# Performance work log

Measured on AMD Instinct MI355X. Metric: run time of the kernel, lower is better.

## Reference

```python
import jax, jax.numpy as jnp
import numpy as np

NUM_HEADS = 16
CAPACITY = 512
ROPE_BASE = 10000.0

def _rope_factor(positions, dim):
    # freqs = exp(linspace(0,-1,dim//2) * log(base)), shape (dim//2,)
    freqs = jnp.exp(jnp.linspace(0.0, -1.0, dim // 2) * jnp.log(jnp.float32(ROPE_BASE)))
    angles = positions[..., None] * freqs            # (..., seq, dim//2)
    return jnp.concatenate([jnp.sin(angles), jnp.cos(angles)], axis=-1)  # (..., seq, dim)

def setup_inputs() -> dict:
    key = jax.random.key(0)
    ks = jax.random.split(key, 6)
    B, Sq, Skv, D = 4, 4096, 4096, 1024
    return {
        "query_seq": jax.random.normal(ks[0], (B, Sq, D), jnp.float32),
        "value_seq": jax.random.normal(ks[1], (B, Skv, D), jnp.float32),
        "router_w": jax.random.normal(ks[2], (1, D), jnp.float32) * 0.02,
        "q_w": jax.random.normal(ks[3], (D, D), jnp.float32) * 0.02,
        "kv_w": jax.random.normal(ks[4], (2 * D, D), jnp.float32) * 0.02,
        "out_w": jax.random.normal(ks[5], (D, D), jnp.float32) * 0.02,
    }

def reference(query_seq, value_seq, router_w, q_w, kv_w, out_w):
    B, Sq, D = query_seq.shape
    Skv = value_seq.shape[1]
    H, C = NUM_HEADS, CAPACITY
    d = D // H

    # router + top-k capacity selection over the sequence dim
    rw = jnp.einsum("bsd,od->bs", query_seq, router_w).astype(jnp.float32)  # (B,Sq)
    top_w, top_idx = jax.lax.top_k(rw, C)                                   # (B,C)

    # gather selected queries
    resampled = jnp.take_along_axis(query_seq, top_idx[:, :, None], axis=1)  # (B,C,D)

    q = jnp.einsum("bcd,ed->bce", resampled, q_w)        # (B,C,H*d)
    kv = jnp.einsum("bsd,ed->bse", value_seq, kv_w)      # (B,Skv,2*H*d)
    k, v = jnp.split(kv, 2, axis=-1)

    q = q.reshape(B, C, H, d).transpose(0, 2, 1, 3)      # (B,H,C,d)
    k = k.reshape(B, Skv, H, d).transpose(0, 2, 1, 3)    # (B,H,Skv,d)
    v = v.reshape(B, Skv, H, d).transpose(0, 2, 1, 3)

    # RoPE-style elementwise modulation (faithful to source: x * cat(sin, cos))
    q_pos = top_idx.astype(jnp.float32)[:, None, :]      # (B,1,C)
    q = q * _rope_factor(q_pos, d)                       # (B,H,C,d)
    k_pos = jnp.arange(Skv, dtype=jnp.float32)[None, :]  # (1,Skv)
    k = k * _rope_factor(k_pos, d)[None]                 # broadcast over (B,H)

    # SDPA
    scores = jnp.einsum("bhcd,bhsd->bhcs", q, k) / jnp.sqrt(jnp.float32(d))
    att = jnp.einsum("bhcs,bhsd->bhcd", jax.nn.softmax(scores, axis=-1), v)

    att = att.transpose(0, 2, 1, 3).reshape(B, C, H * d)  # (B,C,D)
    att = jnp.einsum("bce,de->bcd", att, out_w)           # (B,C,D)

    # weighted scatter back to full sequence
    src = att * top_w[:, :, None]
    out = jnp.zeros_like(query_seq).at[jnp.arange(B)[:, None], top_idx].set(src)
    return out
```

## Files before the change

### kernel.cpp

```cpp
#include <hip/hip_runtime.h>
#include <hip/hip_bf16.h>

#define B_  4
#define SQ  4096
#define SKV 4096
#define DM  1024
#define NH  16
#define HD  64
#define CAP 512

#define ASPLIT 4
#define KVPER  (SKV / ASPLIT)
#define AITERS (KVPER / 64)

typedef __attribute__((ext_vector_type(8))) short    short8;
typedef __attribute__((ext_vector_type(8))) __bf16   bf16v8;
typedef __attribute__((ext_vector_type(4))) float    f32x4;
typedef __attribute__((ext_vector_type(4))) unsigned short ushort4v;

static __device__ __forceinline__ unsigned short f2bf(float f) {
    unsigned u = __float_as_uint(f);
    u += 0x7FFFu + ((u >> 16) & 1u);
    return (unsigned short)(u >> 16);
}

static __device__ __forceinline__ f32x4 mfma_bf16(short8 a, short8 b, f32x4 c) {
    return __builtin_amdgcn_mfma_f32_16x16x32_bf16(
        __builtin_bit_cast(bf16v8, a), __builtin_bit_cast(bf16v8, b), c, 0, 0, 0);
}

#define GLD16(gp, lp)                                                              \
    __builtin_amdgcn_global_load_lds(                                              \
        (__attribute__((address_space(1))) void*)(gp),                             \
        (__attribute__((address_space(3))) void*)(lp), 16, 0, 0)

__global__ void __launch_bounds__(256) k_convert(const float* __restrict__ in,
                                                 unsigned short* __restrict__ out) {
    size_t i = (size_t)blockIdx.x * 256 + threadIdx.x;
    float4 f = ((const float4*)in)[i];
    ushort4v o = { f2bf(f.x), f2bf(f.y), f2bf(f.z), f2bf(f.w) };
    ((ushort4v*)out)[i] = o;
}

__global__ void __launch_bounds__(256) k_rope(float* __restrict__ tab) {
    int g = blockIdx.x * 256 + threadIdx.x;
    int pos = g >> 6, i = g & 63, j = i & 31;
    float freq = expf(-(float)j * (logf(10000.0f) / 31.0f));
    float ang  = (float)pos * freq;
    tab[g] = (i < 32) ? sinf(ang) : cosf(ang);
}

__global__ void __launch_bounds__(256) k_router(const float* __restrict__ q,
                                                const float* __restrict__ wv,
                                                float* __restrict__ rw) {
    int row  = blockIdx.x * 4 + (threadIdx.x >> 6);
    int lane = threadIdx.x & 63;
    const float* p  = q  + (size_t)row * DM + lane * 16;
    const float* wp = wv + lane * 16;
    float s = 0.f;
#pragma unroll
    for (int j = 0; j < 4; j++) {
        float4 a = ((const float4*)p)[j];
        float4 b = ((const float4*)wp)[j];
        s += a.x * b.x + a.y * b.y + a.z * b.z + a.w * b.w;
    }
#pragma unroll
    for (int m = 32; m > 0; m >>= 1) s += __shfl_xor(s, m, 64);
    if (lane == 0) rw[row] = s;
}

__global__ void __launch_bounds__(1024) k_topk(const float* __restrict__ rw,
                                               int* __restrict__ sel,
                                               float* __restrict__ selw) {
    __shared__ unsigned long long keys[4096];
    int b = blockIdx.x, t = threadIdx.x;
    for (int i = t; i < 4096; i += 1024) {
        float v = rw[b * 4096 + i];
        unsigned u = __float_as_uint(v);
        u = (u & 0x80000000u) ? ~u : (u | 0x80000000u);
        keys[i] = ((unsigned long long)(~u) << 32) | (unsigned)i;
    }
    __syncthreads();
    for (int k = 2; k <= 4096; k <<= 1)
        for (int j = k >> 1; j > 0; j >>= 1) {
            for (int i = t; i < 4096; i += 1024) {
                int ixj = i ^ j;
                if (ixj > i) {
                    bool up = ((i & k) == 0);
                    unsigned long long a = keys[i], c = keys[ixj];
                    if ((a > c) == up) { keys[i] = c; keys[ixj] = a; }
                }
            }
            __syncthreads();
        }
    for (int i = t; i < 512; i += 1024) {
        unsigned idx = (unsigned)(keys[i] & 0xFFFFFFFFu);
        sel[b * 512 + i]  = (int)idx;
        selw[b * 512 + i] = rw[b * 4096 + idx];
    }
}

__global__ void __launch_bounds__(256) k_gather(const float* __restrict__ q,
                                                const int* __restrict__ sel,
                                                unsigned short* __restrict__ out) {
    int row = blockIdx.x;
    int b = row >> 9;
    int s = sel[row];
    const float4* src = (const float4*)(q + ((size_t)b * SQ + s) * DM);
    ushort4v* dst = (ushort4v*)(out + (size_t)row * DM);
    float4 f = src[threadIdx.x];
    ushort4v o = { f2bf(f.x), f2bf(f.y), f2bf(f.z), f2bf(f.w) };
    dst[threadIdx.x] = o;
}

template <int MODE, int BN>
__global__ void __launch_bounds__(256) k_gemm(
    const unsigned short* __restrict__ A,
    const unsigned short* __restrict__ Bw,
    int M, int N, int K,
    const float* __restrict__ rope_tab,
    const int* __restrict__ sel,
    const float* __restrict__ selw,
    unsigned short* __restrict__ ok,
    unsigned short* __restrict__ ov,
    unsigned short* __restrict__ obf,
    float* __restrict__ of) {
    constexpr int TN = BN / 32;
    __shared__ unsigned short lA[128 * 32];
    __shared__ unsigned short lB[BN * 32];
    const int tid = threadIdx.x;
    const int w = tid >> 6, lane = tid & 63, quad = lane >> 4, l16 = lane & 15;
    const int wr = w >> 1, wc = w & 1;
    const int mBase = blockIdx.y * 128;
    const int nBase = blockIdx.x * BN + (MODE == 3 ? 1024 : 0);

    f32x4 acc[4][TN] = {};

    for (int k0 = 0; k0 < K; k0 += 32) {
#pragma unroll
        for (int is = 0; is < 2; is++) {
            int slot = is * 256 + tid;
            int row = slot >> 2, sc = slot & 3;
            int kc = (sc - (row >> 1)) & 3;
            const char* ga = (const char*)A + (((size_t)(mBase + row) * K) + k0 + kc * 8) * 2;
            GLD16(ga, (char*)lA + slot * 16);
        }
#pragma unroll
        for (int is = 0; is < BN / 64; is++) {
            int slot = is * 256 + tid;
            int row = slot >> 2, sc = slot & 3;
            int kc = (sc - (row >> 1)) & 3;
            const char* gb = (const char*)Bw + (((size_t)(nBase + row) * K) + k0 + kc * 8) * 2;
            GLD16(gb, (char*)lB + slot * 16);
        }
        __syncthreads();
        short8 af[4], bfr[TN];
#pragma unroll
        for (int t = 0; t < 4; t++) {
            int r = wr * 64 + t * 16 + l16;
            af[t] = *(const short8*)&lA[r * 32 + (((quad + (r >> 1)) & 3) * 8)];
        }
#pragma unroll
        for (int t = 0; t < TN; t++) {
            int r = wc * (BN / 2) + t * 16 + l16;
            bfr[t] = *(const short8*)&lB[r * 32 + (((quad + (r >> 1)) & 3) * 8)];
        }
#pragma unroll
        for (int tm = 0; tm < 4; tm++)
#pragma unroll
            for (int tn = 0; tn < TN; tn++) {
                if constexpr (MODE == 3)
                    acc[tm][tn] = mfma_bf16(bfr[tn], af[tm], acc[tm][tn]);
                else
                    acc[tm][tn] = mfma_bf16(af[tm], bfr[tn], acc[tm][tn]);
            }
        __syncthreads();
    }

#pragma unroll
    for (int tm = 0; tm < 4; tm++) {
#pragma unroll
        for (int tn = 0; tn < TN; tn++) {
#pragma unroll
            for (int r = 0; r < 4; r++) {
                float v = acc[tm][tn][r];
                if constexpr (MODE == 3) {
                    int n = nBase + wc * (BN / 2) + tn * 16 + quad * 4 + r;
                    int m = mBase + wr * 64 + tm * 16 + l16;
                    int e = n - 1024, h = e >> 6, i = e & 63;
                    int b = m >> 12, s = m & 4095;
                    ov[(((size_t)(b * NH + h) * HD) + i) * SKV + s] = f2bf(v);
                } else {
                    int m = mBase + wr * 64 + tm * 16 + quad * 4 + r;
                    int n = nBase + wc * (BN / 2) + tn * 16 + l16;
                    if constexpr (MODE == 0) {
                        int b = m >> 12, s = m & 4095;
                        int h = n >> 6, i = n & 63;
                        v *= rope_tab[(s << 6) | i];
                        ok[(((size_t)(b * NH + h) * SKV) + s) * HD + i] = f2bf(v);
                    } else if constexpr (MODE == 1) {
                        int b = m >> 9, c = m & 511;
                        int h = n >> 6, i = n & 63;
                        float rp = rope_tab[(sel[m] << 6) | i];
                        obf[(((size_t)(b * NH + h) * CAP) + c) * HD + i] =
                            f2bf(v * rp * 0.18033688011112042f);
                    } else {
                        int b = m >> 9;
                        int s = sel[m];
                        of[(((size_t)b * SQ) + s) * DM + n] = v * selw[m];
                    }
                }
            }
        }
    }
}

__global__ void __launch_bounds__(256) k_attention(
    const unsigned short* __restrict__ Q,
    const unsigned short* __restrict__ Kg,
    const unsigned short* __restrict__ Vt,
    float* __restrict__ Opart,
    float* __restrict__ Lpart) {
    __shared__ unsigned short lK[64 * 72];
    __shared__ unsigned short lV[64 * 72];
    __shared__ unsigned short lP[4][32 * 72];
    const int bh = blockIdx.y, z = blockIdx.z;
    const int tid = threadIdx.x, w = tid >> 6, lane = tid & 63;
    const int quad = lane >> 4, l16 = lane & 15;
    const int qb = blockIdx.x * 128 + w * 32;
    const int base = z * KVPER;

    short8 qf[2][2];
#pragma unroll
    for (int rt = 0; rt < 2; rt++) {
        const unsigned short* qp = Q + ((size_t)bh * CAP + qb + rt * 16 + l16) * HD + quad * 8;
        qf[rt][0] = *(const short8*)qp;
        qf[rt][1] = *(const short8*)(qp + 32);
    }

    const unsigned short* kb = Kg + (size_t)bh * SKV * HD;
    const unsigned short* vb = Vt + (size_t)bh * HD * SKV;
    const int sr = tid >> 2, sp = tid & 3;

    f32x4 o[2][4] = {};
    f32x4 lsum[2] = {};
    short8 ones = (short8)0x3F80;

    short8 rk0, rk1, rv0, rv1;
    {
        const short8* srck = (const short8*)(kb + (size_t)(base + sr) * HD + sp * 16);
        rk0 = srck[0]; rk1 = srck[1];
        const short8* srcv = (const short8*)(vb + (size_t)sr * SKV + base + sp * 16);
        rv0 = srcv[0]; rv1 = srcv[1];
    }

    unsigned short* lPw = &lP[w][0];

    for (int it = 0; it < AITERS; it++) {
        __syncthreads();
        *(short8*)&lK[sr * 72 + sp * 16]     = rk0;
        *(short8*)&lK[sr * 72 + sp * 16 + 8] = rk1;
        *(short8*)&lV[sr * 72 + sp * 16]     = rv0;
        *(short8*)&lV[sr * 72 + sp * 16 + 8] = rv1;
        if (it + 1 < AITERS) {
            int s0 = base + (it + 1) * 64;
            const short8* srck = (const short8*)(kb + (size_t)(s0 + sr) * HD + sp * 16);
            rk0 = srck[0]; rk1 = srck[1];
            const short8* srcv = (const short8*)(vb + (size_t)sr * SKV + s0 + sp * 16);
            rv0 = srcv[0]; rv1 = srcv[1];
        }
        __syncthreads();

        f32x4 sc[2][4] = {};
#pragma unroll
        for (int tn = 0; tn < 4; tn++) {
            short8 kf0 = *(const short8*)&lK[(tn * 16 + l16) * 72 + quad * 8];
            short8 kf1 = *(const short8*)&lK[(tn * 16 + l16) * 72 + 32 + quad * 8];
#pragma unroll
            for (int rt = 0; rt < 2; rt++) {
                sc[rt][tn] = mfma_bf16(qf[rt][0], kf0, sc[rt][tn]);
                sc[rt][tn] = mfma_bf16(qf[rt][1], kf1, sc[rt][tn]);
            }
        }
#pragma unroll
        for (int rt = 0; rt < 2; rt++)
#pragma unroll
            for (int tn = 0; tn < 4; tn++)
#pragma unroll
                for (int r = 0; r < 4; r++)
                    lPw[(rt * 16 + quad * 4 + r) * 72 + tn * 16 + l16] =
                        f2bf(exp2f(fminf(sc[rt][tn][r], 86.f)));
#pragma unroll
        for (int kc = 0; kc < 2; kc++) {
            short8 pf0 = *(const short8*)&lPw[(l16) * 72 + kc * 32 + quad * 8];
            short8 pf1 = *(const short8*)&lPw[(16 + l16) * 72 + kc * 32 + quad * 8];
            lsum[0] = mfma_bf16(pf0, ones, lsum[0]);
            lsum[1] = mfma_bf16(pf1, ones, lsum[1]);
#pragma unroll
            for (int tn = 0; tn < 4; tn++) {
                short8 vf = *(const short8*)&lV[(tn * 16 + l16) * 72 + kc * 32 + quad * 8];
                o[0][tn] = mfma_bf16(pf0, vf, o[0][tn]);
                o[1][tn] = mfma_bf16(pf1, vf, o[1][tn]);
            }
        }
    }

    float* Ob = Opart + (((size_t)(z * 64 + bh)) * CAP + qb) * HD;
#pragma unroll
    for (int rt = 0; rt < 2; rt++)
#pragma unroll
        for (int tn = 0; tn < 4; tn++)
#pragma unroll
            for (int r = 0; r < 4; r++)
                Ob[(size_t)(rt * 16 + quad * 4 + r) * HD + tn * 16 + l16] = o[rt][tn][r];
    if (l16 == 0) {
#pragma unroll
        for (int rt = 0; rt < 2; rt++)
#pragma unroll
            for (int r = 0; r < 4; r++)
                Lpart[((size_t)(z * 64 + bh)) * CAP + qb + rt * 16 + quad * 4 + r] = lsum[rt][r];
    }
}

__global__ void __launch_bounds__(256) k_combine(
    const float* __restrict__ Opart, const float* __restrict__ Lpart,
    unsigned short* __restrict__ att) {
    int g = blockIdx.x * 256 + threadIdx.x;
    int dall = g & 1023, c = (g >> 10) & 511, b = g >> 19;
    int h = dall >> 6, dd = dall & 63;
    int bh = b * NH + h;
    float os = 0.f, ls = 0.f;
#pragma unroll
    for (int p = 0; p < ASPLIT; p++) {
        os += Opart[(((size_t)(p * 64 + bh)) * CAP + c) * HD + dd];
        ls += Lpart[((size_t)(p * 64 + bh)) * CAP + c];
    }
    att[g] = f2bf(os / ls);
}

extern "C" void kernel_launch(void* const* d_in, const int* in_sizes, int n_in,
                              void* d_out, int out_size, void* d_ws, size_t ws_size,
                              hipStream_t stream) {
    const float* query    = (const float*)d_in[0];
    const float* value    = (const float*)d_in[1];
    const float* router_w = (const float*)d_in[2];
    const float* q_w      = (const float*)d_in[3];
    const float* kv_w     = (const float*)d_in[4];
    const float* out_w    = (const float*)d_in[5];
    float* out = (float*)d_out;

    char* p = (char*)d_ws;
    unsigned short* value_bf = (unsigned short*)p; p += (size_t)B_ * SKV * DM * 2;
    unsigned short* kvw_bf   = (unsigned short*)p; p += (size_t)2 * DM * DM * 2;
    unsigned short* qw_bf    = (unsigned short*)p; p += (size_t)DM * DM * 2;
    unsigned short* ow_bf    = (unsigned short*)p; p += (size_t)DM * DM * 2;
    unsigned short* res_bf   = (unsigned short*)p; p += (size_t)B_ * CAP * DM * 2;
    unsigned short* q_attn   = (unsigned short*)p; p += (size_t)B_ * CAP * DM * 2;
    unsigned short* kbuf     = (unsigned short*)p; p += (size_t)B_ * SKV * DM * 2;
    unsigned short* vbuf     = (unsigned short*)p; p += (size_t)B_ * SKV * DM * 2;
    unsigned short* att_bf   = (unsigned short*)p; p += (size_t)B_ * CAP * DM * 2;
    float* rope_tab = (float*)p; p += (size_t)SKV * HD * 4;
    float* rw       = (float*)p; p += (size_t)B_ * SQ * 4;
    int*   sel      = (int*)p;   p += (size_t)B_ * CAP * 4;
    float* selw     = (float*)p; p += (size_t)B_ * CAP * 4;
    float* Opart = (float*)value_bf;
    float* Lpart = (float*)res_bf;

    hipMemsetAsync(d_out, 0, (size_t)out_size * sizeof(float), stream);

    k_convert<<<B_ * SKV * DM / 1024, 256, 0, stream>>>(value, value_bf);
    k_convert<<<2 * DM * DM / 1024, 256, 0, stream>>>(kv_w, kvw_bf);
    k_convert<<<DM * DM / 1024, 256, 0, stream>>>(q_w, qw_bf);
    k_convert<<<DM * DM / 1024, 256, 0, stream>>>(out_w, ow_bf);
    k_rope<<<SKV * HD / 256, 256, 0, stream>>>(rope_tab);
    k_router<<<B_ * SQ / 4, 256, 0, stream>>>(query, router_w, rw);
    k_topk<<<B_, 1024, 0, stream>>>(rw, sel, selw);
    k_gather<<<B_ * CAP, 256, 0, stream>>>(query, sel, res_bf);

    k_gemm<0, 128><<<dim3(DM / 128, B_ * SKV / 128), 256, 0, stream>>>(
        value_bf, kvw_bf, B_ * SKV, DM, DM, rope_tab, nullptr, nullptr,
        kbuf, nullptr, nullptr, nullptr);
    k_gemm<3, 128><<<dim3(DM / 128, B_ * SKV / 128), 256, 0, stream>>>(
        value_bf, kvw_bf, B_ * SKV, DM, DM, nullptr, nullptr, nullptr,
        nullptr, vbuf, nullptr, nullptr);
    k_gemm<1, 64><<<dim3(DM / 64, B_ * CAP / 128), 256, 0, stream>>>(
        res_bf, qw_bf, B_ * CAP, DM, DM, rope_tab, sel, nullptr,
        nullptr, nullptr, q_attn, nullptr);

    k_attention<<<dim3(CAP / 128, B_ * NH, ASPLIT), 256, 0, stream>>>(
        q_attn, kbuf, vbuf, Opart, Lpart);
    k_combine<<<B_ * CAP * DM / 256, 256, 0, stream>>>(Opart, Lpart, att_bf);

    k_gemm<2, 64><<<dim3(DM / 64, B_ * CAP / 128), 256, 0, stream>>>(
        att_bf, ow_bf, B_ * CAP, DM, DM, nullptr, sel, selw,
        nullptr, nullptr, nullptr, out);
}
```

Baseline: 492.3 us.

## Keep softmax probabilities in registers instead of staging through LDS

Swaps the operand order of the QK^T MFMA so each lane holds score values in the layout needed for the P·V A operand. The exponentiated scores are then packed to bf16 in registers with v_cvt_pk_bf16_f32, which eliminates the per-wave LDS buffer and its write/read traffic. V fragments are loaded from LDS with a matching k-permutation (two 8-byte reads) so the contraction index lines up with the register-resident P. This cuts LDS bandwidth and shared memory use, at the cost of less vectorized V reads and reliance on inline asm.

Result: no change. 483.6 us (-1.8%).

```diff
diff --git a/kernel.cpp b/kernel.cpp
--- a/kernel.cpp
+++ b/kernel.cpp
@@ -17,6 +17,7 @@
 typedef __attribute__((ext_vector_type(8))) __bf16   bf16v8;
 typedef __attribute__((ext_vector_type(4))) float    f32x4;
 typedef __attribute__((ext_vector_type(4))) unsigned short ushort4v;
+typedef __attribute__((ext_vector_type(4))) unsigned int   uint4v;
 
 static __device__ __forceinline__ unsigned short f2bf(float f) {
     unsigned u = __float_as_uint(f);
@@ -223,7 +224,6 @@
     float* __restrict__ Lpart) {
     __shared__ unsigned short lK[64 * 72];
     __shared__ unsigned short lV[64 * 72];
-    __shared__ unsigned short lP[4][32 * 72];
     const int bh = blockIdx.y, z = blockIdx.z;
     const int tid = threadIdx.x, w = tid >> 6, lane = tid & 63;
     const int quad = lane >> 4, l16 = lane & 15;
@@ -253,8 +253,6 @@
         const short8* srcv = (const short8*)(vb + (size_t)sr * SKV + base + sp * 16);
         rv0 = srcv[0]; rv1 = srcv[1];
     }
-
-    unsigned short* lPw = &lP[w][0];
 
     for (int it = 0; it < AITERS; it++) {
         __syncthreads();
@@ -278,8 +276,8 @@
             short8 kf1 = *(const short8*)&lK[(tn * 16 + l16) * 72 + 32 + quad * 8];
 #pragma unroll
             for (int rt = 0; rt < 2; rt++) {
-                sc[rt][tn] = mfma_bf16(qf[rt][0], kf0, sc[rt][tn]);
-                sc[rt][tn] = mfma_bf16(qf[rt][1], kf1, sc[rt][tn]);
+                sc[rt][tn] = mfma_bf16(kf0, qf[rt][0], sc[rt][tn]);
+                sc[rt][tn] = mfma_bf16(kf1, qf[rt][1], sc[rt][tn]);
             }
         }
 #pragma unroll
@@ -288,19 +286,39 @@
             for (int tn = 0; tn < 4; tn++)
 #pragma unroll
                 for (int r = 0; r < 4; r++)
-                    lPw[(rt * 16 + quad * 4 + r) * 72 + tn * 16 + l16] =
-                        f2bf(exp2f(fminf(sc[rt][tn][r], 86.f)));
+                    sc[rt][tn][r] = exp2f(fminf(sc[rt][tn][r], 86.f));
+
+        short8 pa[2][2];
+#pragma unroll
+        for (int rt = 0; rt < 2; rt++)
+#pragma unroll
+            for (int kc = 0; kc < 2; kc++) {
+                uint4v wv;
+#pragma unroll
+                for (int t = 0; t < 4; t++) {
+                    unsigned pk;
+                    asm("v_cvt_pk_bf16_f32 %0, %1, %2"
+                        : "=v"(pk)
+                        : "v"(sc[rt][kc * 2 + (t >> 1)][(t & 1) * 2]),
+                          "v"(sc[rt][kc * 2 + (t >> 1)][(t & 1) * 2 + 1]));
+                    wv[t] = pk;
+                }
+                pa[rt][kc] = __builtin_bit_cast(short8, wv);
+            }
+
 #pragma unroll
         for (int kc = 0; kc < 2; kc++) {
-            short8 pf0 = *(const short8*)&lPw[(l16) * 72 + kc * 32 + quad * 8];
-            short8 pf1 = *(const short8*)&lPw[(16 + l16) * 72 + kc * 32 + quad * 8];
-            lsum[0] = mfma_bf16(pf0, ones, lsum[0]);
-            lsum[1] = mfma_bf16(pf1, ones, lsum[1]);
+            lsum[0] = mfma_bf16(pa[0][kc], ones, lsum[0]);
+            lsum[1] = mfma_bf16(pa[1][kc], ones, lsum[1]);
 #pragma unroll
             for (int tn = 0; tn < 4; tn++) {
-                short8 vf = *(const short8*)&lV[(tn * 16 + l16) * 72 + kc * 32 + quad * 8];
-                o[0][tn] = mfma_bf16(pf0, vf, o[0][tn]);
-                o[1][tn] = mfma_bf16(pf1, vf, o[1][tn]);
+                const unsigned short* vrow = &lV[(size_t)(tn * 16 + l16) * 72];
+                uint2 g0 = *(const uint2*)(vrow + kc * 32 + quad * 4);
+                uint2 g1 = *(const uint2*)(vrow + kc * 32 + 16 + quad * 4);
+                uint4v wv = { g0.x, g0.y, g1.x, g1.y };
+                short8 vf = __builtin_bit_cast(short8, wv);
+                o[0][tn] = mfma_bf16(pa[0][kc], vf, o[0][tn]);
+                o[1][tn] = mfma_bf16(pa[1][kc], vf, o[1][tn]);
             }
         }
     }
```
